# Kernel optimization log

Hardware: AMD Instinct MI355X
Metric: run time of the kernel (lower is better)

## Reference

```python
import jax, jax.numpy as jnp
import numpy as np

EPS = 1e-12  # F.normalize eps


def _l2norm(v):
    n = jnp.sqrt(jnp.sum(v * v, axis=-1, keepdims=True))
    return v / jnp.maximum(n, EPS)


def setup_inputs() -> dict:
    key = jax.random.key(0)
    ks = jax.random.split(key, 6)
    B, S, D, F, E = 2, 2048, 1024, 4096, 8
    std = 0.02
    return {
        "x": jax.random.normal(ks[0], (B, S, D), jnp.float32),
        "Wp": jax.random.normal(ks[1], (D, D), jnp.float32) * (1.0 / np.sqrt(D)),
        "sim_matrix": jax.random.normal(ks[2], (E, D), jnp.float32) * std,
        "temperature": jnp.asarray(1.0, jnp.float32),
        "W1": jax.random.normal(ks[3], (E, D, F), jnp.float32) * (1.0 / np.sqrt(D)),
        "b1": jnp.zeros((E, F), jnp.float32),
        "W2": jax.random.normal(ks[4], (E, F, D), jnp.float32) * (1.0 / np.sqrt(F)),
        "b2": jnp.zeros((E, D), jnp.float32),
    }


def reference(x, Wp, sim_matrix, temperature, W1, b1, W2, b2):
    # ---- cosine gate ----
    E = sim_matrix.shape[0]
    top_k = 2
    proj = jnp.einsum("bsd,ed->bse", x, Wp)            # Linear(d,d), weight [out,in]
    pn = _l2norm(proj)                                   # [B,S,D]
    sn = _l2norm(sim_matrix)                             # [E,D]
    gate_scores = jnp.einsum("bsd,ed->bse", pn, sn) / temperature
    top_v, top_i = jax.lax.top_k(gate_scores, top_k)     # [B,S,K]
    gate_probs = jax.nn.softmax(top_v, axis=-1)          # [B,S,K]
    # per-token combine weight per expert: sum_k prob_k * 1[idx_k==e]
    comb = jnp.sum(jax.nn.one_hot(top_i, E, dtype=x.dtype) * gate_probs[..., None], axis=-2)  # [B,S,E]
    # ---- experts (dense over all experts, masked combine = original math) ----
    h = jax.nn.gelu(jnp.einsum("bsd,edf->ebsf", x, W1) + b1[:, None, None, :], approximate=False)
    eo = jnp.einsum("ebsf,efd->ebsd", h, W2) + b2[:, None, None, :]  # [E,B,S,D]
    out = jnp.einsum("ebsd,bse->bsd", eo, comb)
    return out
```

## Files before the change

### kernel.cpp

```cpp
#include <hip/hip_runtime.h>
#include <hip/hip_bf16.h>
#include <math.h>

#define NTOK 4096
#define DD 1024
#define FF 4096
#define NEXP 8
#define EBM 128
#define EBN 128
#define EBK 32
#define PAIR_CAP 9216
#define TILES_MAX 72

typedef short bf16x8 __attribute__((ext_vector_type(8)));
typedef float f32x4 __attribute__((ext_vector_type(4)));
typedef unsigned short u16x8 __attribute__((ext_vector_type(8)));

__device__ __forceinline__ ushort f2bf(float x) {
  unsigned u = __float_as_uint(x);
  unsigned r = (u + 0x7FFFu + ((u >> 16) & 1u)) >> 16;
  return (ushort)r;
}

__device__ __forceinline__ void async16(const void* g, void* l) {
  __builtin_amdgcn_global_load_lds(
      (const __attribute__((address_space(1))) char*)g,
      (__attribute__((address_space(3))) char*)l, 16, 0, 0);
}


__global__ void k_convert4(const float4* __restrict__ s, ushort* __restrict__ d, int n4) {
  int i = blockIdx.x * 256 + threadIdx.x;
  if (i >= n4) return;
  float4 v = s[i];
  ushort4 o;
  o.x = f2bf(v.x); o.y = f2bf(v.y); o.z = f2bf(v.z); o.w = f2bf(v.w);
  *(ushort4*)(d + (size_t)i * 4) = o;
}

__global__ void k_transpose(const float* __restrict__ src, ushort* __restrict__ dst,
                            int R, int C) {
  __shared__ float tile[128][65];
  int e = blockIdx.z;
  const float* s = src + (size_t)e * R * C;
  ushort* d = dst + (size_t)e * R * C;
  int c0 = blockIdx.x * 64, r0 = blockIdx.y * 128;
  int tid = threadIdx.x;
  int rr0 = tid >> 4;
  int cc4 = (tid & 15) * 4;
#pragma unroll
  for (int ps = 0; ps < 8; ++ps) {
    int r = ps * 16 + rr0;
    float4 v = *(const float4*)&s[(size_t)(r0 + r) * C + c0 + cc4];
    tile[r][cc4 + 0] = v.x; tile[r][cc4 + 1] = v.y;
    tile[r][cc4 + 2] = v.z; tile[r][cc4 + 3] = v.w;
  }
  __syncthreads();
  int cw = tid >> 4;
  int rp = (tid & 15) * 8;
#pragma unroll
  for (int pass = 0; pass < 4; ++pass) {
    int c = pass * 16 + cw;
    u16x8 o;
#pragma unroll
    for (int k = 0; k < 8; ++k) o[k] = f2bf(tile[rp + k][c]);
    *(u16x8*)&d[(size_t)(c0 + c) * R + r0 + rp] = o;
  }
}

__global__ void k_simnorm(const float* __restrict__ sim, double* __restrict__ snorm) {
  int wid = threadIdx.x >> 6, lane = threadIdx.x & 63;
  double s = 0.0;
  for (int d = lane; d < DD; d += 64) { double v = sim[wid * DD + d]; s += v * v; }
#pragma unroll
  for (int m = 32; m; m >>= 1) s += __shfl_down(s, m);
  if (lane == 0) snorm[wid] = sqrt(s);
}

__global__ void k_u(const float* __restrict__ wp, const float* __restrict__ sim,
                    const double* __restrict__ snorm, double* __restrict__ u) {
  int d = blockIdx.x * 256 + threadIdx.x;
  int e = blockIdx.y;
  double acc = 0.0;
#pragma unroll 8
  for (int o = 0; o < DD; ++o)
    acc += (double)wp[(size_t)o * DD + d] * (double)sim[e * DD + o];
  u[e * DD + d] = acc / fmax(snorm[e], 1e-12);
}

__global__ void k_nured(const float* __restrict__ part, float* __restrict__ nu) {
  int t = blockIdx.x * 256 + threadIdx.x;
  float s = 0.f;
#pragma unroll
  for (int i = 0; i < 16; ++i) s += part[t * 16 + i];
  nu[t] = s;
}

__global__ void k_gate(const float* __restrict__ x, const double* __restrict__ u,
                       const float* __restrict__ nu, const float* __restrict__ temp,
                       int* __restrict__ t2e, float* __restrict__ t2p) {
  int wid = threadIdx.x >> 6, lane = threadIdx.x & 63;
  int t = blockIdx.x * 4 + wid;
  double acc[NEXP];
#pragma unroll
  for (int e = 0; e < NEXP; ++e) acc[e] = 0.0;
  for (int d = lane; d < DD; d += 64) {
    double xv = x[(size_t)t * DD + d];
#pragma unroll
    for (int e = 0; e < NEXP; ++e) acc[e] += xv * u[e * DD + d];
  }
#pragma unroll
  for (int e = 0; e < NEXP; ++e)
    for (int m = 32; m; m >>= 1) acc[e] += __shfl_down(acc[e], m);
  if (lane == 0) {
    double den = fmax(sqrt((double)nu[t]), 1e-12) * (double)temp[0];
    double s[NEXP];
#pragma unroll
    for (int e = 0; e < NEXP; ++e) s[e] = acc[e] / den;
    int e1 = 0; double v1 = s[0];
    for (int e = 1; e < NEXP; ++e) if (s[e] > v1) { v1 = s[e]; e1 = e; }
    int e2 = -1; double v2 = -1e300;
    for (int e = 0; e < NEXP; ++e) if (e != e1 && s[e] > v2) { v2 = s[e]; e2 = e; }
    double z = exp(v2 - v1);
    double inv = 1.0 / (1.0 + z);
    t2e[t * 2] = e1; t2e[t * 2 + 1] = e2;
    t2p[t * 2] = (float)inv; t2p[t * 2 + 1] = (float)(z * inv);
  }
}

__global__ void k_count(const int* __restrict__ t2e, int* __restrict__ meta,
                        int* __restrict__ ptok, float* __restrict__ pp) {
  __shared__ int cnt[NEXP];
  int tid = threadIdx.x;
  if (tid < NEXP) cnt[tid] = 0;
  __syncthreads();
  for (int i = tid; i < NTOK * 2; i += 256) atomicAdd(&cnt[t2e[i]], 1);
  __syncthreads();
  if (tid == 0) {
    int off = 0;
    for (int e = 0; e < NEXP; ++e) {
      meta[e] = cnt[e];
      meta[8 + e] = off;
      off += ((cnt[e] + EBM - 1) / EBM) * EBM;
    }
    meta[16] = off;
    meta[17] = off / EBM;
    for (int e = 0; e < NEXP; ++e) meta[18 + e] = 0;
    int ti = 0;
    for (int e = 0; e < NEXP; ++e) {
      int nt = (cnt[e] + EBM - 1) / EBM;
      for (int k = 0; k < nt; ++k) meta[26 + ti++] = e;
    }
  }
  for (int i = tid; i < PAIR_CAP; i += 256) { ptok[i] = 0; pp[i] = 0.f; }
}

__global__ void k_scatter(const int* __restrict__ t2e, const float* __restrict__ t2p,
                          int* __restrict__ meta, int* __restrict__ ptok,
                          float* __restrict__ pp) {
  int i = blockIdx.x * 256 + threadIdx.x;
  if (i >= NTOK * 2) return;
  int e = t2e[i];
  int slot = atomicAdd(&meta[18 + e], 1);
  int pos = meta[8 + e] + slot;
  ptok[pos] = i >> 1;
  pp[pos] = t2p[i];
}

template <int EPI>
__launch_bounds__(256, 4)
__global__ void gemm_x(const ushort* __restrict__ Abase, const ushort* __restrict__ Bbase,
                       int K, int Brows,
                       const int* __restrict__ pair_tok, const float* __restrict__ pair_p,
                       const int* __restrict__ meta, const float* __restrict__ bias,
                       float* __restrict__ nu_part, ushort* __restrict__ hout,
                       float* __restrict__ outp, int g_tiles, int nby, int tile0) {
  __shared__ ushort As[2][EBM * EBK];
  __shared__ ushort Bs[2][EBN * EBK];
  __shared__ int tok_s[EBM];
  __shared__ float p_s[EBM];

  const int tid = threadIdx.x;
  const int lane = tid & 63;
  const int wid = tid >> 6;

  int tile, nb;
  {
    int bid = blockIdx.x;
    if ((g_tiles & 1) == 0 && (nby & 3) == 0) {
      int x = bid & 7, b = bid >> 3;
      int i = x >> 2, j = x & 3;
      int nt = g_tiles >> 1, np = nby >> 2;
      int t_loc = b / np, p_loc = b - t_loc * np;
      tile = i * nt + t_loc;
      nb = j * np + p_loc;
    } else {
      tile = bid % g_tiles;
      nb = bid / g_tiles;
    }
  }
  tile += tile0;

  int expert = 0;
  if constexpr (EPI != 0) {
    if (tile >= meta[17]) return;
    expert = meta[26 + tile];
    if (tid < EBM) {
      int pr = tile * EBM + tid;
      tok_s[tid] = pair_tok[pr];
      p_s[tid] = pair_p[pr];
    }
    __syncthreads();
  }

  const char* Ac = (const char*)Abase;
  const char* Bc = (const char*)(Bbase + (size_t)expert * Brows * K);

  const char* asrc[2];
  const char* bsrc[2];
#pragma unroll
  for (int i = 0; i < 2; ++i) {
    int c = i * 256 + tid;
    int m = c >> 2, cc = c & 3;
    int sw = (cc ^ (m & 3)) << 4;
    int arow;
    if constexpr (EPI == 1) arow = tok_s[m];
    else if constexpr (EPI == 2) arow = (tile - tile0) * EBM + m;
    else arow = tile * EBM + m;
    asrc[i] = Ac + (size_t)arow * K * 2 + sw;
    bsrc[i] = Bc + (size_t)(nb * EBN + m) * K * 2 + sw;
  }

  const int wr = wid >> 1, wc = wid & 1;
  const int l15 = lane & 15, lg = lane >> 4;

  f32x4 acc[4][4];
#pragma unroll
  for (int a = 0; a < 4; ++a)
#pragma unroll
    for (int b = 0; b < 4; ++b) acc[a][b] = (f32x4){0.f, 0.f, 0.f, 0.f};

  const int nk = K / EBK;

#pragma unroll
  for (int i = 0; i < 2; ++i) {
    async16(asrc[i], (char*)(&As[0][0]) + (i * 256 + wid * 64) * 16);
    async16(bsrc[i], (char*)(&Bs[0][0]) + (i * 256 + wid * 64) * 16);
  }

  for (int kt = 0; kt < nk; ++kt) {
    const int cur = kt & 1;
    __syncthreads();
    if (kt + 1 < nk) {
      const size_t ko = (size_t)(kt + 1) * EBK * 2;
#pragma unroll
      for (int i = 0; i < 2; ++i) {
        async16(asrc[i] + ko, (char*)(&As[cur ^ 1][0]) + (i * 256 + wid * 64) * 16);
        async16(bsrc[i] + ko, (char*)(&Bs[cur ^ 1][0]) + (i * 256 + wid * 64) * 16);
      }
    }
    const char* Ab = (const char*)(&As[cur][0]);
    const char* Bb = (const char*)(&Bs[cur][0]);
    bf16x8 af[4], bfr[4];
#pragma unroll
    for (int fi = 0; fi < 4; ++fi) {
      int r = wr * 64 + fi * 16 + l15;
      int cidx = lg ^ (r & 3);
      af[fi] = *(const bf16x8*)(Ab + r * 64 + cidx * 16);
    }
#pragma unroll
    for (int fj = 0; fj < 4; ++fj) {
      int r = wc * 64 + fj * 16 + l15;
      int cidx = lg ^ (r & 3);
      bfr[fj] = *(const bf16x8*)(Bb + r * 64 + cidx * 16);
    }
#pragma unroll
    for (int fi = 0; fi < 4; ++fi)
#pragma unroll
      for (int fj = 0; fj < 4; ++fj)
        acc[fi][fj] =
            __builtin_amdgcn_mfma_f32_16x16x32_bf16(af[fi], bfr[fj], acc[fi][fj], 0, 0, 0);
  }

  if constexpr (EPI == 0) {
#pragma unroll
    for (int fi = 0; fi < 4; ++fi) {
#pragma unroll
      for (int j = 0; j < 4; ++j) {
        float s = 0.f;
#pragma unroll
        for (int fj = 0; fj < 4; ++fj) { float v = acc[fi][fj][j]; s += v * v; }
        s += __shfl_xor(s, 1); s += __shfl_xor(s, 2);
        s += __shfl_xor(s, 4); s += __shfl_xor(s, 8);
        if (l15 == 0) {
          int row = tile * EBM + wr * 64 + fi * 16 + lg * 4 + j;
          nu_part[row * 16 + nb * 2 + wc] = s;
        }
      }
    }
  } else if constexpr (EPI == 1) {
    float bv[4];
#pragma unroll
    for (int fj = 0; fj < 4; ++fj)
      bv[fj] = bias[expert * FF + nb * EBN + wc * 64 + fj * 16 + l15];
#pragma unroll
    for (int fi = 0; fi < 4; ++fi)
#pragma unroll
      for (int fj = 0; fj < 4; ++fj)
#pragma unroll
        for (int j = 0; j < 4; ++j) {
          float v = acc[fi][fj][j] + bv[fj];
          float g = 0.5f * v * (1.0f + erff(v * 0.70710678118654752f));
          int rl = wr * 64 + fi * 16 + lg * 4 + j;
          size_t grow = (size_t)(tile - tile0) * EBM + rl;
          int col = nb * EBN + wc * 64 + fj * 16 + l15;
          hout[grow * FF + col] = f2bf(g);
        }
  } else {
    float bv[4];
#pragma unroll
    for (int fj = 0; fj < 4; ++fj)
      bv[fj] = bias[expert * DD + nb * EBN + wc * 64 + fj * 16 + l15];
#pragma unroll
    for (int fi = 0; fi < 4; ++fi) {
      int rl = wr * 64 + fi * 16 + lg * 4;
#pragma unroll
      for (int j = 0; j < 4; ++j) {
        int tok = tok_s[rl + j];
        float p = p_s[rl + j];
#pragma unroll
        for (int fj = 0; fj < 4; ++fj) {
          float v = (acc[fi][fj][j] + bv[fj]) * p;
          int col = nb * EBN + wc * 64 + fj * 16 + l15;
          atomicAdd(outp + (size_t)tok * DD + col, v);
        }
      }
    }
  }
}


extern "C" void kernel_launch(void* const* d_in, const int* in_sizes, int n_in,
                              void* d_out, int out_size, void* d_ws, size_t ws_size,
                              hipStream_t stream) {
  const float* x = (const float*)d_in[0];
  const float* wp = (const float*)d_in[1];
  const float* sim = (const float*)d_in[2];
  const float* temp = (const float*)d_in[3];
  const float* w1 = (const float*)d_in[4];
  const float* b1 = (const float*)d_in[5];
  const float* w2 = (const float*)d_in[6];
  const float* b2 = (const float*)d_in[7];
  float* out = (float*)d_out;

  char* w = (char*)d_ws;
  size_t off = 0;
  auto alloc = [&](size_t sz) {
    char* p = w + off;
    off = (off + sz + 255) & ~(size_t)255;
    return p;
  };
  double* u = (double*)alloc((size_t)NEXP * DD * 8);
  double* snorm = (double*)alloc(NEXP * 8);
  float* nu_part = (float*)alloc((size_t)NTOK * 16 * 4);
  float* nu = (float*)alloc((size_t)NTOK * 4);
  int* t2e = (int*)alloc((size_t)NTOK * 2 * 4);
  float* t2p = (float*)alloc((size_t)NTOK * 2 * 4);
  int* meta = (int*)alloc(512);
  int* ptok = (int*)alloc((size_t)PAIR_CAP * 4);
  float* pp = (float*)alloc((size_t)PAIR_CAP * 4);
  ushort* xbf = (ushort*)alloc((size_t)NTOK * DD * 2);
  ushort* wpbf = (ushort*)alloc((size_t)DD * DD * 2);
  ushort* w1t = (ushort*)alloc((size_t)NEXP * DD * FF * 2);
  ushort* w2t = (ushort*)alloc((size_t)NEXP * DD * FF * 2);
  size_t havail = (ws_size > off) ? (ws_size - off) : 0;
  int G = (int)(havail / ((size_t)EBM * FF * 2));
  if (G > TILES_MAX) G = TILES_MAX;
  if (G >= 8) G &= ~7;
  if (G < 1) G = 1;
  ushort* h = (ushort*)(w + off);

  hipMemsetAsync(d_out, 0, (size_t)out_size * 4, stream);

  k_convert4<<<dim3(NTOK * DD / 4 / 256), 256, 0, stream>>>((const float4*)x, xbf, NTOK * DD / 4);
  k_convert4<<<dim3(DD * DD / 4 / 256), 256, 0, stream>>>((const float4*)wp, wpbf, DD * DD / 4);
  k_transpose<<<dim3(FF / 64, DD / 128, NEXP), 256, 0, stream>>>(w1, w1t, DD, FF);
  k_transpose<<<dim3(DD / 64, FF / 128, NEXP), 256, 0, stream>>>(w2, w2t, FF, DD);
  k_simnorm<<<1, 512, 0, stream>>>(sim, snorm);
  k_u<<<dim3(DD / 256, NEXP), 256, 0, stream>>>(wp, sim, snorm, u);
  gemm_x<0><<<dim3((NTOK / EBM) * (DD / EBN)), 256, 0, stream>>>(
      xbf, wpbf, DD, DD, nullptr, nullptr, nullptr, nullptr, nu_part, nullptr, nullptr,
      NTOK / EBM, DD / EBN, 0);
  k_nured<<<dim3(NTOK / 256), 256, 0, stream>>>(nu_part, nu);
  k_gate<<<dim3(NTOK / 4), 256, 0, stream>>>(x, u, nu, temp, t2e, t2p);
  k_count<<<1, 256, 0, stream>>>(t2e, meta, ptok, pp);
  k_scatter<<<dim3(NTOK * 2 / 256), 256, 0, stream>>>(t2e, t2p, meta, ptok, pp);

  for (int t0 = 0; t0 < TILES_MAX; t0 += G) {
    int g = TILES_MAX - t0;
    if (g > G) g = G;
    gemm_x<1><<<dim3(g * (FF / EBN)), 256, 0, stream>>>(
        xbf, w1t, DD, FF, ptok, pp, meta, b1, nullptr, h, nullptr, g, FF / EBN, t0);
    gemm_x<2><<<dim3(g * (DD / EBN)), 256, 0, stream>>>(
        h, w2t, FF, DD, ptok, pp, meta, b2, nullptr, nullptr, out, g, DD / EBN, t0);
  }
}
```

Before: 545.8 us.

## Add wider 128x256 tile kernel for expert up-projection and change LDS swizzle

Replaces the first expert GEMM (x·W1 with GELU) with a new 512-thread kernel that computes 128x256 output tiles, so each gathered A tile is reused across twice as many columns. It also remaps block IDs so that blocks sharing tiles run close together, which should improve L2 reuse. The LDS XOR swizzle changes from row&3 to (row>>1)&3 in both kernels to cut bank conflicts on the 16-byte fragment reads. The wider tile uses more shared memory and registers per block, which can lower occupancy, and partial tiles in the grid may leave some waves idle.

```diff
diff --git a/kernel.cpp b/kernel.cpp
--- a/kernel.cpp
+++ b/kernel.cpp
@@ -222,17 +222,18 @@
   for (int i = 0; i < 2; ++i) {
     int c = i * 256 + tid;
     int m = c >> 2, cc = c & 3;
-    int sw = (cc ^ (m & 3)) << 4;
+    int sw = (cc ^ ((m >> 1) & 3)) << 4;
     int arow;
-    if constexpr (EPI == 1) arow = tok_s[m];
-    else if constexpr (EPI == 2) arow = (tile - tile0) * EBM + m;
+    if constexpr (EPI == 2) arow = (tile - tile0) * EBM + m;
     else arow = tile * EBM + m;
+    if constexpr (EPI == 2) (void)0;
     asrc[i] = Ac + (size_t)arow * K * 2 + sw;
     bsrc[i] = Bc + (size_t)(nb * EBN + m) * K * 2 + sw;
   }
 
   const int wr = wid >> 1, wc = wid & 1;
   const int l15 = lane & 15, lg = lane >> 4;
+  const int fxor = (l15 >> 1) & 3;
 
   f32x4 acc[4][4];
 #pragma unroll
@@ -265,13 +266,13 @@
 #pragma unroll
     for (int fi = 0; fi < 4; ++fi) {
       int r = wr * 64 + fi * 16 + l15;
-      int cidx = lg ^ (r & 3);
+      int cidx = lg ^ fxor;
       af[fi] = *(const bf16x8*)(Ab + r * 64 + cidx * 16);
     }
 #pragma unroll
     for (int fj = 0; fj < 4; ++fj) {
       int r = wc * 64 + fj * 16 + l15;
-      int cidx = lg ^ (r & 3);
+      int cidx = lg ^ fxor;
       bfr[fj] = *(const bf16x8*)(Bb + r * 64 + cidx * 16);
     }
 #pragma unroll
@@ -298,24 +299,6 @@
         }
       }
     }
-  } else if constexpr (EPI == 1) {
-    float bv[4];
-#pragma unroll
-    for (int fj = 0; fj < 4; ++fj)
-      bv[fj] = bias[expert * FF + nb * EBN + wc * 64 + fj * 16 + l15];
-#pragma unroll
-    for (int fi = 0; fi < 4; ++fi)
-#pragma unroll
-      for (int fj = 0; fj < 4; ++fj)
-#pragma unroll
-        for (int j = 0; j < 4; ++j) {
-          float v = acc[fi][fj][j] + bv[fj];
-          float g = 0.5f * v * (1.0f + erff(v * 0.70710678118654752f));
-          int rl = wr * 64 + fi * 16 + lg * 4 + j;
-          size_t grow = (size_t)(tile - tile0) * EBM + rl;
-          int col = nb * EBN + wc * 64 + fj * 16 + l15;
-          hout[grow * FF + col] = f2bf(g);
-        }
   } else {
     float bv[4];
 #pragma unroll
@@ -337,6 +320,127 @@
       }
     }
   }
+}
+
+__launch_bounds__(512, 4)
+__global__ void gemm_w(const ushort* __restrict__ Abase, const ushort* __restrict__ Bbase,
+                       int K, const int* __restrict__ pair_tok, const float* __restrict__ pair_p,
+                       const int* __restrict__ meta, const float* __restrict__ bias,
+                       ushort* __restrict__ hout, int g_tiles, int nby, int tile0) {
+  __shared__ ushort As[2][128 * EBK];
+  __shared__ ushort Bs[2][256 * EBK];
+  __shared__ int tok_s[128];
+
+  const int tid = threadIdx.x;
+  const int lane = tid & 63;
+  const int wid = tid >> 6;
+
+  int tile, nb;
+  {
+    int bid = blockIdx.x;
+    if ((g_tiles & 1) == 0 && (nby & 3) == 0) {
+      int x = bid & 7, b = bid >> 3;
+      int i = x >> 2, j = x & 3;
+      int nt = g_tiles >> 1, np = nby >> 2;
+      int t_loc = b / np, p_loc = b - t_loc * np;
+      tile = i * nt + t_loc;
+      nb = j * np + p_loc;
+    } else {
+      tile = bid % g_tiles;
+      nb = bid / g_tiles;
+    }
+  }
+  tile += tile0;
+
+  if (tile >= meta[17]) return;
+  const int expert = meta[26 + tile];
+  if (tid < 128) tok_s[tid] = pair_tok[tile * 128 + tid];
+  __syncthreads();
+
+  const char* Ac = (const char*)Abase;
+  const char* Bc = (const char*)(Bbase + (size_t)expert * FF * K);
+
+  const char* asrc;
+  {
+    int m = tid >> 2, cc = tid & 3;
+    int sw = (cc ^ ((m >> 1) & 3)) << 4;
+    asrc = Ac + (size_t)tok_s[m] * K * 2 + sw;
+  }
+  const char* bsrc[2];
+#pragma unroll
+  for (int i = 0; i < 2; ++i) {
+    int c = i * 512 + tid;
+    int m = c >> 2, cc = c & 3;
+    int sw = (cc ^ ((m >> 1) & 3)) << 4;
+    bsrc[i] = Bc + (size_t)(nb * 256 + m) * K * 2 + sw;
+  }
+
+  const int wr = wid >> 2, wc = wid & 3;
+  const int l15 = lane & 15, lg = lane >> 4;
+  const int fxor = (l15 >> 1) & 3;
+
+  f32x4 acc[4][4];
+#pragma unroll
+  for (int a = 0; a < 4; ++a)
+#pragma unroll
+    for (int b = 0; b < 4; ++b) acc[a][b] = (f32x4){0.f, 0.f, 0.f, 0.f};
+
+  const int nk = K / EBK;
+  char* AsB = (char*)(&As[0][0]);
+  char* BsB = (char*)(&Bs[0][0]);
+
+  async16(asrc, AsB + wid * 1024);
+#pragma unroll
+  for (int i = 0; i < 2; ++i) async16(bsrc[i], BsB + i * 8192 + wid * 1024);
+
+  for (int kt = 0; kt < nk; ++kt) {
+    const int cur = kt & 1;
+    __syncthreads();
+    if (kt + 1 < nk) {
+      const size_t ko = (size_t)(kt + 1) * EBK * 2;
+      async16(asrc + ko, AsB + (cur ^ 1) * 8192 + wid * 1024);
+#pragma unroll
+      for (int i = 0; i < 2; ++i)
+        async16(bsrc[i] + ko, BsB + (cur ^ 1) * 16384 + i * 8192 + wid * 1024);
+    }
+    const char* Ab = AsB + cur * 8192;
+    const char* Bb = BsB + cur * 16384;
+    bf16x8 af[4], bfr[4];
+#pragma unroll
+    for (int fi = 0; fi < 4; ++fi) {
+      int r = wr * 64 + fi * 16 + l15;
+      af[fi] = *(const bf16x8*)(Ab + r * 64 + (lg ^ fxor) * 16);
+    }
+#pragma unroll
+    for (int fj = 0; fj < 4; ++fj) {
+      int r = wc * 64 + fj * 16 + l15;
+      bfr[fj] = *(const bf16x8*)(Bb + r * 64 + (lg ^ fxor) * 16);
+    }
+#pragma unroll
+    for (int fi = 0; fi < 4; ++fi)
+#pragma unroll
+      for (int fj = 0; fj < 4; ++fj)
+        acc[fi][fj] =
+            __builtin_amdgcn_mfma_f32_16x16x32_bf16(af[fi], bfr[fj], acc[fi][fj], 0, 0, 0);
+  }
+
+  float bv[4];
+#pragma unroll
+  for (int fj = 0; fj < 4; ++fj)
+    bv[fj] = bias[expert * FF + nb * 256 + wc * 64 + fj * 16 + l15];
+#pragma unroll
+  for (int fi = 0; fi < 4; ++fi)
+#pragma unroll
+    for (int fj = 0; fj < 4; ++fj)
+#pragma unroll
+      for (int j = 0; j < 4; ++j) {
+        float v = acc[fi][fj][j] + bv[fj];
+        float g = 0.5f * v * (1.0f + erff(v * 0.70710678118654752f));
+        int rl = wr * 64 + fi * 16 + lg * 4 + j;
+        size_t grow = (size_t)(tile - tile0) * 128 + rl;
+        int col = nb * 256 + wc * 64 + fj * 16 + l15;
+        hout[grow * FF + col] = f2bf(g);
+      }
 }
 
 
@@ -399,8 +503,8 @@
   for (int t0 = 0; t0 < TILES_MAX; t0 += G) {
     int g = TILES_MAX - t0;
     if (g > G) g = G;
-    gemm_x<1><<<dim3(g * (FF / EBN)), 256, 0, stream>>>(
-        xbf, w1t, DD, FF, ptok, pp, meta, b1, nullptr, h, nullptr, g, FF / EBN, t0);
+    gemm_w<<<dim3(g * (FF / 256)), 512, 0, stream>>>(
+        xbf, w1t, DD, ptok, pp, meta, b1, h, g, FF / 256, t0);
     gemm_x<2><<<dim3(g * (DD / EBN)), 256, 0, stream>>>(
         h, w2t, FF, DD, ptok, pp, meta, b2, nullptr, nullptr, out, g, DD / EBN, t0);
   }
```

New measurement: 550.3 us. No clear change (+0.8%).
